# Optimization experiments

Hardware: AMD Instinct MI355X
Metric: run time of the kernel (lower is better)

## Reference

```python
import jax, jax.numpy as jnp
import numpy as np

H = 64        # hidden_dim
A = 21        # N_ACTIONS
B = 262144    # batch size


def setup_inputs() -> dict:
    key = jax.random.key(0)
    ks = jax.random.split(key, 32)

    def w(k, shape):
        fan_in = shape[0]
        return (jax.random.normal(k, shape, jnp.float32) / np.float32(np.sqrt(fan_in)))

    inp = {
        "x": jax.random.normal(ks[0], (B, 2, 2), jnp.float32),
        "b_act1": jax.random.randint(ks[1], (B,), 0, A),
        "b_act2": jax.random.randint(ks[2], (B,), 0, A),
        # enc: Linear(2,H), ReLU, Linear(H,H), ReLU
        "enc_w1": w(ks[3], (2, H)), "enc_b1": jnp.zeros((H,), jnp.float32),
        "enc_w2": w(ks[4], (H, H)), "enc_b2": jnp.zeros((H,), jnp.float32),
        # q_net: Linear(H,H), ReLU, Linear(H,A)
        "q_w1": w(ks[5], (H, H)), "q_b1": jnp.zeros((H,), jnp.float32),
        "q_w2": w(ks[6], (H, A)), "q_b2": jnp.zeros((A,), jnp.float32),
        # v_net: Linear(H,H), ReLU, Linear(H,1)
        "v_w1": w(ks[7], (H, H)), "v_b1": jnp.zeros((H,), jnp.float32),
        "v_w2": w(ks[8], (H, 1)), "v_b2": jnp.zeros((1,), jnp.float32),
        # lin2: Linear(H+A,H), ReLU, Linear(H,H), ReLU, Linear(H,H)
        "l2_w1": w(ks[9], (H + A, H)), "l2_b1": jnp.zeros((H,), jnp.float32),
        "l2_w2": w(ks[10], (H, H)), "l2_b2": jnp.zeros((H,), jnp.float32),
        "l2_w3": w(ks[11], (H, H)), "l2_b3": jnp.zeros((H,), jnp.float32),
        # lin3, lin4
        "l3_w": w(ks[12], (H, H)), "l3_b": jnp.zeros((H,), jnp.float32),
        "l4_w": w(ks[13], (H, A)), "l4_b": jnp.zeros((A,), jnp.float32),
        # q_prime_net: Linear(H,2H) ELU Linear(2H,H) ELU Linear(H,H) ELU Linear(H,1)
        "qp_w1": w(ks[14], (H, 2 * H)), "qp_b1": jnp.zeros((2 * H,), jnp.float32),
        "qp_w2": w(ks[15], (2 * H, H)), "qp_b2": jnp.zeros((H,), jnp.float32),
        "qp_w3": w(ks[16], (H, H)), "qp_b3": jnp.zeros((H,), jnp.float32),
        "qp_w4": w(ks[17], (H, 1)), "qp_b4": jnp.zeros((1,), jnp.float32),
    }
    return inp


def reference(x, b_act1, b_act2,
              enc_w1, enc_b1, enc_w2, enc_b2,
              q_w1, q_b1, q_w2, q_b2,
              v_w1, v_b1, v_w2, v_b2,
              l2_w1, l2_b1, l2_w2, l2_b2, l2_w3, l2_b3,
              l3_w, l3_b, l4_w, l4_b,
              qp_w1, qp_b1, qp_w2, qp_b2, qp_w3, qp_b3, qp_w4, qp_b4):
    relu = jax.nn.relu
    elu = jax.nn.elu

    def enc(z):
        return relu(relu(z @ enc_w1 + enc_b1) @ enc_w2 + enc_b2)

    def q_net(h):
        return relu(h @ q_w1 + q_b1) @ q_w2 + q_b2

    def lin2(e):  # ends with bare Linear (no final activation)
        h = relu(e @ l2_w1 + l2_b1)
        h = relu(h @ l2_w2 + l2_b2)
        return h @ l2_w3 + l2_b3

    def q_prime(z):
        h = elu(z @ qp_w1 + qp_b1)
        h = elu(h @ qp_w2 + qp_b2)
        h = elu(h @ qp_w3 + qp_b3)
        return h @ qp_w4 + qp_b4

    h1 = enc(x[:, 0, :])  # [B,H]
    h2 = enc(x[:, 1, :])
    q1, q2 = q_net(h1), q_net(h2)              # [B,A]
    key2 = jnp.stack([h1, h2], axis=1)          # [B,2,H]
    vtot = relu((h1 + h2) @ v_w1 + v_b1) @ v_w2 + v_b2  # [B,1]

    def joint(act1, act2):
        oh1 = jax.nn.one_hot(act1, A, dtype=h1.dtype)
        oh2 = jax.nn.one_hot(act2, A, dtype=h2.dtype)
        e = jnp.stack([jnp.concatenate([h1, oh1], axis=-1),
                       jnp.concatenate([h2, oh2], axis=-1)], axis=1)  # [B,2,H+A]
        key1 = lin2(e)                              # [B,2,H]
        q = q_prime(key1.mean(axis=1))              # [B,1]
        return key1, q

    key1, joint_qs = joint(b_act1, b_act2)
    a1_max = jnp.argmax(q1, axis=1)
    a2_max = jnp.argmax(q2, axis=1)
    key1_max, joint_max_qs = joint(a1_max, a2_max)

    def q_jt(k1):
        z = key2 + k1.mean(axis=1, keepdims=True) - k1 / 2  # [B,2,H]
        return relu(z @ l3_w + l3_b) @ l4_w + l4_b           # [B,2,A]

    q_jt_alt = q_jt(key1)
    q_jt_max_alt = q_jt(key1_max)

    return (q1, q2, joint_qs, joint_max_qs, vtot, q_jt_alt, q_jt_max_alt)
```

## Files before the change

### kernel.cpp

```cpp
#include <hip/hip_runtime.h>
#include <hip/hip_bf16.h>


#define B_TOT 262144

typedef __bf16 bf16_t;
typedef __bf16 bf16x4 __attribute__((ext_vector_type(4)));
typedef __bf16 bf16x8 __attribute__((ext_vector_type(8)));
typedef float  f32x2  __attribute__((ext_vector_type(2)));
typedef float  f32x4  __attribute__((ext_vector_type(4)));

#define MFMA16(a, b, c) __builtin_amdgcn_mfma_f32_16x16x32_bf16((a), (b), (c), 0, 0, 0)

enum : int {
  OFF_VW1  = 0,
  OFF_L2W1 = 4096,
  OFF_L2W2 = 8192,
  OFF_L2W3 = 12288,
  OFF_L3W  = 16384,
  OFF_L4W  = 20480,
  OFF_QP1  = 22528,
  OFF_QP2  = 30720,
  OFF_QP3  = 38912,
  WS_ELEMS = 43008
};
#define WS_BYTES (WS_ELEMS * 2)

enum : int {
  O_Q1   = 0,
  O_Q2   = 21 * B_TOT,
  O_JQ   = 42 * B_TOT,
  O_JMQ  = 43 * B_TOT,
  O_VT   = 44 * B_TOT,
  O_QJT  = 45 * B_TOT,
  O_QJTM = 87 * B_TOT
};

struct RDesc { const float* src; int K; int N; int NT; int off; };
struct RPack { RDesc d[9]; };

__global__ void repack_kernel(RPack P, bf16_t* __restrict__ ws) {
  RDesc d = P.d[blockIdx.x];
  int n = (d.K >> 5) * d.NT * 512;
  for (int i = threadIdx.x; i < n; i += blockDim.x) {
    int j  = i & 7;
    int l  = (i >> 3) & 63;
    int t  = i >> 9;
    int nt = t % d.NT;
    int kc = t / d.NT;
    int sk = kc * 32 + 16 * (j >> 2) + 4 * (l >> 4) + (j & 3);
    int sn = nt * 16 + (l & 15);
    float v = (sn < d.N) ? d.src[sk * d.N + sn] : 0.0f;
    ws[d.off + i] = (bf16_t)v;
  }
}

struct Args {
  const float* x; const int* a1; const int* a2;
  const float* ew1; const float* eb1; const float* ew2; const float* eb2;
  const float* qw1; const float* qb1; const float* qw2; const float* qb2;
  const float* vw1; const float* vb1; const float* vw2; const float* vb2;
  const float* l2w1; const float* l2b1; const float* l2w2; const float* l2b2;
  const float* l2w3; const float* l2b3;
  const float* l3w;  const float* l3b;  const float* l4w;  const float* l4b;
  const float* qpw1; const float* qpb1; const float* qpw2; const float* qpb2;
  const float* qpw3; const float* qpb3; const float* qpw4; const float* qpb4;
  float* out; const bf16_t* ws;
};

struct __align__(16) SMem {
  bf16_t h1b[64 * 72];
  bf16_t h2b[64 * 72];
  unsigned char scr[34816];
  float  bias[768];
  bf16_t oneh[21 * 68];
  int    acts[128];
  int    amax[128];
  float  red[64][2];
  int    redi[64][2];
};

__device__ __forceinline__ float eluf(float x) { return x > 0.f ? x : expm1f(x); }

__device__ __forceinline__ void fcA64(const float* __restrict__ fin, float* __restrict__ fout,
                                      const float* __restrict__ W, const float* __restrict__ Bv,
                                      bf16_t* hb, int r, int g) {
  f32x2 acc[8];
  const f32x2* Bv2 = (const f32x2*)(Bv + g * 16);
#pragma unroll
  for (int i = 0; i < 8; i++) acc[i] = Bv2[i];
#pragma unroll 4
  for (int k4 = 0; k4 < 16; k4++) {
    float4 a = *(const float4*)(fin + r * 68 + k4 * 4);
    float av[4] = {a.x, a.y, a.z, a.w};
#pragma unroll
    for (int kk = 0; kk < 4; kk++) {
      const f32x2* wr = (const f32x2*)(W + (k4 * 4 + kk) * 64 + g * 16);
      f32x2 avv = {av[kk], av[kk]};
#pragma unroll
      for (int i = 0; i < 8; i++) acc[i] += avv * wr[i];
    }
  }
#pragma unroll
  for (int i = 0; i < 8; i++) {
    float v0 = fmaxf(acc[i][0], 0.f), v1 = fmaxf(acc[i][1], 0.f);
    f32x2 v = {v0, v1};
    *(f32x2*)(fout + r * 68 + g * 16 + 2 * i) = v;
    if (hb) {
      hb[r * 72 + g * 16 + 2 * i]     = (bf16_t)v0;
      hb[r * 72 + g * 16 + 2 * i + 1] = (bf16_t)v1;
    }
  }
}

template <int NC>
__device__ __forceinline__ void qn2(const float* __restrict__ fin, const float* __restrict__ W21,
                                    const float* __restrict__ Bv, float* __restrict__ qo,
                                    int r, int colbase, float& bv, int& bi) {
  float acc[NC];
#pragma unroll
  for (int i = 0; i < NC; i++) acc[i] = Bv[colbase + i];
  for (int k4 = 0; k4 < 16; k4++) {
    float4 a = *(const float4*)(fin + r * 68 + k4 * 4);
    float av[4] = {a.x, a.y, a.z, a.w};
#pragma unroll
    for (int kk = 0; kk < 4; kk++) {
      const float* wr = W21 + (k4 * 4 + kk) * 21 + colbase;
#pragma unroll
      for (int i = 0; i < NC; i++) acc[i] = fmaf(av[kk], wr[i], acc[i]);
    }
  }
  bv = -3e38f; bi = 0;
#pragma unroll
  for (int i = 0; i < NC; i++) {
    qo[i] = acc[i];
    if (acc[i] > bv) { bv = acc[i]; bi = colbase + i; }
  }
}

template <bool USEWS, int NT, int KC>
__device__ __forceinline__ f32x4 tileT(const bf16x8* __restrict__ WF,
                                       const float* __restrict__ Wp, int N, int woff,
                                       const bf16x8* __restrict__ bin,
                                       const float* __restrict__ bias, int bbase,
                                       int nt, int l, int c, int u) {
  f32x4 a = *(const f32x4*)(bias + bbase + nt * 16 + 4 * u);
#pragma unroll
  for (int kc = 0; kc < KC; kc++) {
    bf16x8 w;
    if constexpr (USEWS) {
      w = WF[(woff >> 3) + (kc * NT + nt) * 64 + l];
    } else {
      int sn = nt * 16 + c;
      if (sn < N) {
#pragma unroll
        for (int j = 0; j < 8; j++)
          w[j] = (bf16_t)Wp[(kc * 32 + 16 * (j >> 2) + 4 * u + (j & 3)) * N + sn];
      } else {
#pragma unroll
        for (int j = 0; j < 8; j++) w[j] = (bf16_t)0.0f;
      }
    }
    a = MFMA16(w, bin[kc], a);
  }
  return a;
}

template <int MODE>
__device__ __forceinline__ bf16x8 pack2(f32x4 t0, f32x4 t1) {
  bf16x8 r;
#pragma unroll
  for (int j = 0; j < 8; j++) {
    float v = (j >> 2) ? t1[j & 3] : t0[j & 3];
    if constexpr (MODE == 1) v = fmaxf(v, 0.f);
    if constexpr (MODE == 2) v = eluf(v);
    r[j] = (bf16_t)v;
  }
  return r;
}

template <bool USEWS>
__global__ __launch_bounds__(256, 2) void qtran_main(Args A) {
  __shared__ SMem sm;
  const int t = threadIdx.x;
  const int wgbase = blockIdx.x * 64;
  const int r = t & 63;
  const int g = __builtin_amdgcn_readfirstlane(t >> 6);

  float* f0 = (float*)sm.scr;
  float* f1 = f0 + 64 * 68;

  if (t < 64) {
    sm.bias[t]        = A.vb1[t];
    sm.bias[64 + t]   = A.l2b1[t];
    sm.bias[128 + t]  = A.l2b2[t];
    sm.bias[192 + t]  = A.l2b3[t];
    sm.bias[384 + t]  = A.qpb2[t];
    sm.bias[448 + t]  = A.qpb3[t];
    sm.bias[512 + t]  = A.l3b[t];
    sm.bias[608 + t]  = A.vw2[t];
    sm.bias[672 + t]  = A.qpw4[t];
    sm.acts[t]        = A.a1[wgbase + t];
    sm.acts[64 + t]   = A.a2[wgbase + t];
  } else if (t < 192) {
    sm.bias[256 + t - 64] = A.qpb1[t - 64];
  } else if (t < 224) {
    int i = t - 192;
    sm.bias[576 + i] = (i < 21) ? A.l4b[i] : 0.0f;
  } else if (t == 224) {
    sm.bias[736] = A.vb2[0];
    sm.bias[737] = A.qpb4[0];
  }
  for (int i = t; i < 21 * 68; i += 256) {
    int a_ = i / 68, n_ = i % 68;
    sm.oneh[i] = (bf16_t)((n_ < 64) ? A.l2w1[(64 + a_) * 64 + n_] : 0.0f);
  }

  const int rowg = wgbase + r;
  float4 xv = ((const float4*)A.x)[rowg];
#pragma unroll 1
  for (int s = 0; s < 2; ++s) {
    float xa = s ? xv.z : xv.x;
    float xb = s ? xv.w : xv.y;
#pragma unroll
    for (int cc = 0; cc < 16; cc++) {
      int col = g * 16 + cc;
      float h = fmaf(xa, A.ew1[col], fmaf(xb, A.ew1[64 + col], A.eb1[col]));
      f0[r * 68 + col] = fmaxf(h, 0.f);
    }
    __syncthreads();
    fcA64(f0, f1, A.ew2, A.eb2, s ? sm.h2b : sm.h1b, r, g);
    __syncthreads();
    fcA64(f1, f0, A.qw1, A.qb1, nullptr, r, g);
    __syncthreads();
    {
      float* qo = A.out + (s ? O_Q2 : O_Q1) + rowg * 21;
      float bv; int bi;
      if (g == 0) {
        qn2<16>(f0, A.qw2, A.qb2, qo, r, 0, bv, bi);
        sm.red[r][0] = bv; sm.redi[r][0] = bi;
      } else if (g == 1) {
        qn2<5>(f0, A.qw2, A.qb2, qo + 16, r, 16, bv, bi);
        sm.red[r][1] = bv; sm.redi[r][1] = bi;
      }
    }
    __syncthreads();
    if (t < 64)
      sm.amax[s * 64 + t] = (sm.red[t][0] >= sm.red[t][1]) ? sm.redi[t][0] : sm.redi[t][1];
    __syncthreads();
  }
  __syncthreads();

  const int l = t & 63;
  const int c = l & 15, u = l >> 4;
  const int rb = g * 16;
  const int row = rb + c;
  float* out = A.out;
  const bf16x8* WF = (const bf16x8*)A.ws;
  const float* bias = sm.bias;
  float* S = (float*)sm.scr;

  auto HG = [&](const bf16_t* __restrict__ HB, int kc) -> bf16x8 {
    const bf16_t* p = HB + row * 72 + kc * 32 + 4 * u;
    bf16x4 lo = *(const bf16x4*)p;
    bf16x4 hi = *(const bf16x4*)(p + 16);
    bf16x8 rr;
#pragma unroll
    for (int d = 0; d < 4; d++) { rr[d] = lo[d]; rr[4 + d] = hi[d]; }
    return rr;
  };

  {
    bf16x8 aS[2];
#pragma unroll
    for (int kc = 0; kc < 2; kc++) {
      bf16x8 a1 = HG(sm.h1b, kc), a2 = HG(sm.h2b, kc);
      bf16x8 s8;
#pragma unroll
      for (int i = 0; i < 8; i++) s8[i] = (bf16_t)((float)a1[i] + (float)a2[i]);
      aS[kc] = s8;
    }
    float pr = 0.f;
#pragma unroll
    for (int nt = 0; nt < 4; nt++) {
      f32x4 tv = tileT<USEWS, 4, 2>(WF, A.vw1, 64, OFF_VW1, aS, bias, 0, nt, l, c, u);
      f32x4 wv = *(const f32x4*)(bias + 608 + nt * 16 + 4 * u);
#pragma unroll
      for (int p = 0; p < 4; p++) pr += fmaxf(tv[p], 0.f) * wv[p];
    }
    pr += __shfl_xor(pr, 16, 64);
    pr += __shfl_xor(pr, 32, 64);
    if (u == 0) out[O_VT + wgbase + row] = pr + bias[736];
  }

  const int* actsrc[2] = {sm.acts, sm.amax};
  bf16x8 k1f[2][2][2];
  f32x4 msum[2][4];

#pragma unroll
  for (int j = 0; j < 2; j++) {
    const bf16_t* HB = j ? sm.h2b : sm.h1b;
    bf16x8 bh[2];
#pragma unroll
    for (int kc = 0; kc < 2; kc++) bh[kc] = HG(HB, kc);
    f32x4 tS[4];
#pragma unroll
    for (int nt = 0; nt < 4; nt++)
      tS[nt] = tileT<USEWS, 4, 2>(WF, A.l2w1, 64, OFF_L2W1, bh, bias, 64, nt, l, c, u);
    bf16x8 b1[2][2];
#pragma unroll
    for (int x = 0; x < 2; x++) {
      const int act = actsrc[x][j * 64 + row];
      f32x4 tt0 = tS[0], tt1 = tS[1], tt2 = tS[2], tt3 = tS[3];
      bf16x4 oh0 = *(const bf16x4*)(sm.oneh + act * 68 + 0 * 16 + 4 * u);
      bf16x4 oh1 = *(const bf16x4*)(sm.oneh + act * 68 + 1 * 16 + 4 * u);
      bf16x4 oh2 = *(const bf16x4*)(sm.oneh + act * 68 + 2 * 16 + 4 * u);
      bf16x4 oh3 = *(const bf16x4*)(sm.oneh + act * 68 + 3 * 16 + 4 * u);
#pragma unroll
      for (int p = 0; p < 4; p++) {
        tt0[p] += (float)oh0[p]; tt1[p] += (float)oh1[p];
        tt2[p] += (float)oh2[p]; tt3[p] += (float)oh3[p];
      }
      b1[x][0] = pack2<1>(tt0, tt1);
      b1[x][1] = pack2<1>(tt2, tt3);
    }
    bf16x8 b2[2][2];
#pragma unroll
    for (int x = 0; x < 2; x++)
#pragma unroll
      for (int f = 0; f < 2; f++) {
        f32x4 t0 = tileT<USEWS, 4, 2>(WF, A.l2w2, 64, OFF_L2W2, b1[x], bias, 128, 2 * f, l, c, u);
        f32x4 t1 = tileT<USEWS, 4, 2>(WF, A.l2w2, 64, OFF_L2W2, b1[x], bias, 128, 2 * f + 1, l, c, u);
        b2[x][f] = pack2<1>(t0, t1);
      }
#pragma unroll
    for (int x = 0; x < 2; x++)
#pragma unroll
      for (int f = 0; f < 2; f++) {
        f32x4 t0 = tileT<USEWS, 4, 2>(WF, A.l2w3, 64, OFF_L2W3, b2[x], bias, 192, 2 * f, l, c, u);
        f32x4 t1 = tileT<USEWS, 4, 2>(WF, A.l2w3, 64, OFF_L2W3, b2[x], bias, 192, 2 * f + 1, l, c, u);
        k1f[x][j][f] = pack2<0>(t0, t1);
        if (j == 0) { msum[x][2 * f] = t0; msum[x][2 * f + 1] = t1; }
        else        { msum[x][2 * f] += t0; msum[x][2 * f + 1] += t1; }
      }
  }

#pragma unroll
  for (int j = 0; j < 2; j++) {
    const bf16_t* HB = j ? sm.h2b : sm.h1b;
    bf16x8 h8[2];
#pragma unroll
    for (int kc = 0; kc < 2; kc++) h8[kc] = HG(HB, kc);
#pragma unroll
    for (int x = 0; x < 2; x++) {
      bf16x8 aZ[2];
#pragma unroll
      for (int kc = 0; kc < 2; kc++) {
        bf16x8 kk = k1f[x][1 - j][kc];
#pragma unroll
        for (int i = 0; i < 8; i++)
          aZ[kc][i] = (bf16_t)((float)h8[kc][i] + 0.5f * (float)kk[i]);
      }
      bf16x8 bz[2];
#pragma unroll
      for (int f = 0; f < 2; f++) {
        f32x4 t0 = tileT<USEWS, 4, 2>(WF, A.l3w, 64, OFF_L3W, aZ, bias, 512, 2 * f, l, c, u);
        f32x4 t1 = tileT<USEWS, 4, 2>(WF, A.l3w, 64, OFF_L3W, aZ, bias, 512, 2 * f + 1, l, c, u);
        bz[f] = pack2<1>(t0, t1);
      }
#pragma unroll
      for (int nt = 0; nt < 2; nt++) {
        f32x4 tq = tileT<USEWS, 2, 2>(WF, A.l4w, 21, OFF_L4W, bz, bias, 576, nt, l, c, u);
#pragma unroll
        for (int p = 0; p < 4; p++) {
          int n2 = nt * 16 + 4 * u + p;
          if (n2 < 21) S[x * 2752 + row * 43 + j * 21 + n2] = tq[p];
        }
      }
    }
  }

  {
    bf16x8 aM[2][2];
#pragma unroll
    for (int x = 0; x < 2; x++)
#pragma unroll
      for (int kc = 0; kc < 2; kc++) {
        f32x4 m0 = 0.5f * msum[x][2 * kc], m1 = 0.5f * msum[x][2 * kc + 1];
        aM[x][kc] = pack2<0>(m0, m1);
      }
    bf16x8 bq[2][4];
#pragma unroll
    for (int x = 0; x < 2; x++)
#pragma unroll
      for (int f = 0; f < 4; f++) {
        f32x4 t0 = tileT<USEWS, 8, 2>(WF, A.qpw1, 128, OFF_QP1, aM[x], bias, 256, 2 * f, l, c, u);
        f32x4 t1 = tileT<USEWS, 8, 2>(WF, A.qpw1, 128, OFF_QP1, aM[x], bias, 256, 2 * f + 1, l, c, u);
        bq[x][f] = pack2<2>(t0, t1);
      }
    bf16x8 b3[2][2];
#pragma unroll
    for (int x = 0; x < 2; x++)
#pragma unroll
      for (int f = 0; f < 2; f++) {
        f32x4 t0 = tileT<USEWS, 4, 4>(WF, A.qpw2, 64, OFF_QP2, bq[x], bias, 384, 2 * f, l, c, u);
        f32x4 t1 = tileT<USEWS, 4, 4>(WF, A.qpw2, 64, OFF_QP2, bq[x], bias, 384, 2 * f + 1, l, c, u);
        b3[x][f] = pack2<2>(t0, t1);
      }
    float pj[2] = {0.f, 0.f};
#pragma unroll
    for (int x = 0; x < 2; x++)
#pragma unroll
      for (int nt = 0; nt < 4; nt++) {
        f32x4 tq = tileT<USEWS, 4, 2>(WF, A.qpw3, 64, OFF_QP3, b3[x], bias, 448, nt, l, c, u);
        f32x4 w4 = *(const f32x4*)(bias + 672 + nt * 16 + 4 * u);
#pragma unroll
        for (int p = 0; p < 4; p++) pj[x] += eluf(tq[p]) * w4[p];
      }
#pragma unroll
    for (int x = 0; x < 2; x++) {
      float v = pj[x];
      v += __shfl_xor(v, 16, 64);
      v += __shfl_xor(v, 32, 64);
      if (u == 0) out[(x ? O_JMQ : O_JQ) + wgbase + row] = v + bias[737];
    }
  }

#pragma unroll
  for (int x = 0; x < 2; x++) {
    const int ob = (x ? O_QJTM : O_QJT) + (wgbase + rb) * 42;
    const float* Sx = S + x * 2752 + rb * 43;
    for (int i2 = l; i2 < 672; i2 += 64)
      out[ob + i2] = Sx[(i2 / 42) * 43 + (i2 % 42)];
  }
}

extern "C" void kernel_launch(void* const* d_in, const int* in_sizes, int n_in,
                              void* d_out, int out_size, void* d_ws, size_t ws_size,
                              hipStream_t stream) {
  (void)in_sizes; (void)n_in; (void)out_size;
  Args A;
  A.x    = (const float*)d_in[0];
  A.a1   = (const int*)d_in[1];
  A.a2   = (const int*)d_in[2];
  A.ew1  = (const float*)d_in[3];
  A.eb1  = (const float*)d_in[4];
  A.ew2  = (const float*)d_in[5];
  A.eb2  = (const float*)d_in[6];
  A.qw1  = (const float*)d_in[7];
  A.qb1  = (const float*)d_in[8];
  A.qw2  = (const float*)d_in[9];
  A.qb2  = (const float*)d_in[10];
  A.vw1  = (const float*)d_in[11];
  A.vb1  = (const float*)d_in[12];
  A.vw2  = (const float*)d_in[13];
  A.vb2  = (const float*)d_in[14];
  A.l2w1 = (const float*)d_in[15];
  A.l2b1 = (const float*)d_in[16];
  A.l2w2 = (const float*)d_in[17];
  A.l2b2 = (const float*)d_in[18];
  A.l2w3 = (const float*)d_in[19];
  A.l2b3 = (const float*)d_in[20];
  A.l3w  = (const float*)d_in[21];
  A.l3b  = (const float*)d_in[22];
  A.l4w  = (const float*)d_in[23];
  A.l4b  = (const float*)d_in[24];
  A.qpw1 = (const float*)d_in[25];
  A.qpb1 = (const float*)d_in[26];
  A.qpw2 = (const float*)d_in[27];
  A.qpb2 = (const float*)d_in[28];
  A.qpw3 = (const float*)d_in[29];
  A.qpb3 = (const float*)d_in[30];
  A.qpw4 = (const float*)d_in[31];
  A.qpb4 = (const float*)d_in[32];
  A.out  = (float*)d_out;
  A.ws   = (const bf16_t*)d_ws;

  if (ws_size >= (size_t)WS_BYTES) {
    bf16_t* ws = (bf16_t*)d_ws;
    RPack P;
    P.d[0] = {A.vw1,  64, 64,  4, OFF_VW1};
    P.d[1] = {A.l2w1, 64, 64,  4, OFF_L2W1};
    P.d[2] = {A.l2w2, 64, 64,  4, OFF_L2W2};
    P.d[3] = {A.l2w3, 64, 64,  4, OFF_L2W3};
    P.d[4] = {A.l3w,  64, 64,  4, OFF_L3W};
    P.d[5] = {A.l4w,  64, 21,  2, OFF_L4W};
    P.d[6] = {A.qpw1, 64, 128, 8, OFF_QP1};
    P.d[7] = {A.qpw2, 128, 64, 4, OFF_QP2};
    P.d[8] = {A.qpw3, 64, 64,  4, OFF_QP3};
    hipLaunchKernelGGL(repack_kernel, dim3(9), dim3(256), 0, stream, P, ws);
    hipLaunchKernelGGL(HIP_KERNEL_NAME(qtran_main<true>), dim3(B_TOT / 64), dim3(256), 0,
                       stream, A);
  } else {
    hipLaunchKernelGGL(HIP_KERNEL_NAME(qtran_main<false>), dim3(B_TOT / 64), dim3(256), 0,
                       stream, A);
  }
}
```

Measured before the change: 908.0 us.

## Shrink LDS footprint and raise occupancy to four workgroups per CU

Cuts shared memory by running the encoder/q-net FC layers in place in one float buffer (stride 66), tightening the bf16 hidden buffers to stride 68, and dropping the LDS one-hot table in favour of direct global reads of l2_w1 rows. The q_jt output staging is reordered so each x pass writes out before the next, which halves the S scratch. The launch bound is raised to 4 blocks per CU so more waves can hide latency. In exchange, the in-place FC adds extra barriers and register staging, and the tighter register budget may cause spills.

```diff
diff --git a/kernel.cpp b/kernel.cpp
--- a/kernel.cpp
+++ b/kernel.cpp
@@ -69,11 +69,10 @@
 };
 
 struct __align__(16) SMem {
-  bf16_t h1b[64 * 72];
-  bf16_t h2b[64 * 72];
-  unsigned char scr[34816];
+  unsigned char scr[16896];
+  bf16_t h1b[64 * 68];
+  bf16_t h2b[64 * 68];
   float  bias[768];
-  bf16_t oneh[21 * 68];
   int    acts[128];
   int    amax[128];
   float  red[64][2];
@@ -82,35 +81,45 @@
 
 __device__ __forceinline__ float eluf(float x) { return x > 0.f ? x : expm1f(x); }
 
-__device__ __forceinline__ void fcA64(const float* __restrict__ fin, float* __restrict__ fout,
-                                      const float* __restrict__ W, const float* __restrict__ Bv,
-                                      bf16_t* hb, int r, int g) {
+__device__ __forceinline__ void fcA64ip(float* __restrict__ f,
+                                        const float* __restrict__ W,
+                                        const float* __restrict__ Bv,
+                                        bf16_t* __restrict__ hb, int r, int g) {
   f32x2 acc[8];
   const f32x2* Bv2 = (const f32x2*)(Bv + g * 16);
 #pragma unroll
   for (int i = 0; i < 8; i++) acc[i] = Bv2[i];
+  const f32x2* fr = (const f32x2*)(f + r * 66);
+#pragma unroll 1
+  for (int hh = 0; hh < 2; hh++) {
+    f32x2 in[16];
+#pragma unroll
+    for (int i = 0; i < 16; i++) in[i] = fr[16 * hh + i];
 #pragma unroll 4
-  for (int k4 = 0; k4 < 16; k4++) {
-    float4 a = *(const float4*)(fin + r * 68 + k4 * 4);
-    float av[4] = {a.x, a.y, a.z, a.w};
-#pragma unroll
-    for (int kk = 0; kk < 4; kk++) {
-      const f32x2* wr = (const f32x2*)(W + (k4 * 4 + kk) * 64 + g * 16);
-      f32x2 avv = {av[kk], av[kk]};
-#pragma unroll
-      for (int i = 0; i < 8; i++) acc[i] += avv * wr[i];
-    }
-  }
+    for (int k2 = 0; k2 < 16; k2++) {
+      int k = 32 * hh + 2 * k2;
+      const f32x2* wr0 = (const f32x2*)(W + k * 64 + g * 16);
+      const f32x2* wr1 = (const f32x2*)(W + (k + 1) * 64 + g * 16);
+      f32x2 a0 = {in[k2][0], in[k2][0]};
+      f32x2 a1 = {in[k2][1], in[k2][1]};
+#pragma unroll
+      for (int i = 0; i < 8; i++) acc[i] += a0 * wr0[i];
+#pragma unroll
+      for (int i = 0; i < 8; i++) acc[i] += a1 * wr1[i];
+    }
+  }
+  __syncthreads();
 #pragma unroll
   for (int i = 0; i < 8; i++) {
     float v0 = fmaxf(acc[i][0], 0.f), v1 = fmaxf(acc[i][1], 0.f);
     f32x2 v = {v0, v1};
-    *(f32x2*)(fout + r * 68 + g * 16 + 2 * i) = v;
+    *(f32x2*)(f + r * 66 + g * 16 + 2 * i) = v;
     if (hb) {
-      hb[r * 72 + g * 16 + 2 * i]     = (bf16_t)v0;
-      hb[r * 72 + g * 16 + 2 * i + 1] = (bf16_t)v1;
-    }
-  }
+      hb[r * 68 + g * 16 + 2 * i]     = (bf16_t)v0;
+      hb[r * 68 + g * 16 + 2 * i + 1] = (bf16_t)v1;
+    }
+  }
+  __syncthreads();
 }
 
 template <int NC>
@@ -120,15 +129,14 @@
   float acc[NC];
 #pragma unroll
   for (int i = 0; i < NC; i++) acc[i] = Bv[colbase + i];
-  for (int k4 = 0; k4 < 16; k4++) {
-    float4 a = *(const float4*)(fin + r * 68 + k4 * 4);
-    float av[4] = {a.x, a.y, a.z, a.w};
-#pragma unroll
-    for (int kk = 0; kk < 4; kk++) {
-      const float* wr = W21 + (k4 * 4 + kk) * 21 + colbase;
-#pragma unroll
-      for (int i = 0; i < NC; i++) acc[i] = fmaf(av[kk], wr[i], acc[i]);
-    }
+  for (int k2 = 0; k2 < 32; k2++) {
+    f32x2 a = *(const f32x2*)(fin + r * 66 + 2 * k2);
+    const float* wr0 = W21 + (2 * k2) * 21 + colbase;
+    const float* wr1 = W21 + (2 * k2 + 1) * 21 + colbase;
+#pragma unroll
+    for (int i = 0; i < NC; i++) acc[i] = fmaf(a[0], wr0[i], acc[i]);
+#pragma unroll
+    for (int i = 0; i < NC; i++) acc[i] = fmaf(a[1], wr1[i], acc[i]);
   }
   bv = -3e38f; bi = 0;
 #pragma unroll
@@ -180,7 +188,7 @@
 }
 
 template <bool USEWS>
-__global__ __launch_bounds__(256, 2) void qtran_main(Args A) {
+__global__ __launch_bounds__(256, 4) void qtran_main(Args A) {
   __shared__ SMem sm;
   const int t = threadIdx.x;
   const int wgbase = blockIdx.x * 64;
@@ -188,7 +196,6 @@
   const int g = __builtin_amdgcn_readfirstlane(t >> 6);
 
   float* f0 = (float*)sm.scr;
-  float* f1 = f0 + 64 * 68;
 
   if (t < 64) {
     sm.bias[t]        = A.vb1[t];
@@ -211,10 +218,6 @@
     sm.bias[736] = A.vb2[0];
     sm.bias[737] = A.qpb4[0];
   }
-  for (int i = t; i < 21 * 68; i += 256) {
-    int a_ = i / 68, n_ = i % 68;
-    sm.oneh[i] = (bf16_t)((n_ < 64) ? A.l2w1[(64 + a_) * 64 + n_] : 0.0f);
-  }
 
   const int rowg = wgbase + r;
   float4 xv = ((const float4*)A.x)[rowg];
@@ -223,16 +226,16 @@
     float xa = s ? xv.z : xv.x;
     float xb = s ? xv.w : xv.y;
 #pragma unroll
-    for (int cc = 0; cc < 16; cc++) {
+    for (int cc = 0; cc < 16; cc += 2) {
       int col = g * 16 + cc;
-      float h = fmaf(xa, A.ew1[col], fmaf(xb, A.ew1[64 + col], A.eb1[col]));
-      f0[r * 68 + col] = fmaxf(h, 0.f);
+      float h0 = fmaf(xa, A.ew1[col],     fmaf(xb, A.ew1[64 + col],     A.eb1[col]));
+      float h1 = fmaf(xa, A.ew1[col + 1], fmaf(xb, A.ew1[64 + col + 1], A.eb1[col + 1]));
+      f32x2 v = {fmaxf(h0, 0.f), fmaxf(h1, 0.f)};
+      *(f32x2*)(f0 + r * 66 + col) = v;
     }
     __syncthreads();
-    fcA64(f0, f1, A.ew2, A.eb2, s ? sm.h2b : sm.h1b, r, g);
-    __syncthreads();
-    fcA64(f1, f0, A.qw1, A.qb1, nullptr, r, g);
-    __syncthreads();
+    fcA64ip(f0, A.ew2, A.eb2, s ? sm.h2b : sm.h1b, r, g);
+    fcA64ip(f0, A.qw1, A.qb1, nullptr, r, g);
     {
       float* qo = A.out + (s ? O_Q2 : O_Q1) + rowg * 21;
       float bv; int bi;
@@ -249,7 +252,6 @@
       sm.amax[s * 64 + t] = (sm.red[t][0] >= sm.red[t][1]) ? sm.redi[t][0] : sm.redi[t][1];
     __syncthreads();
   }
-  __syncthreads();
 
   const int l = t & 63;
   const int c = l & 15, u = l >> 4;
@@ -261,7 +263,7 @@
   float* S = (float*)sm.scr;
 
   auto HG = [&](const bf16_t* __restrict__ HB, int kc) -> bf16x8 {
-    const bf16_t* p = HB + row * 72 + kc * 32 + 4 * u;
+    const bf16_t* p = HB + row * 68 + kc * 32 + 4 * u;
     bf16x4 lo = *(const bf16x4*)p;
     bf16x4 hi = *(const bf16x4*)(p + 16);
     bf16x8 rr;
@@ -311,16 +313,11 @@
 #pragma unroll
     for (int x = 0; x < 2; x++) {
       const int act = actsrc[x][j * 64 + row];
-      f32x4 tt0 = tS[0], tt1 = tS[1], tt2 = tS[2], tt3 = tS[3];
-      bf16x4 oh0 = *(const bf16x4*)(sm.oneh + act * 68 + 0 * 16 + 4 * u);
-      bf16x4 oh1 = *(const bf16x4*)(sm.oneh + act * 68 + 1 * 16 + 4 * u);
-      bf16x4 oh2 = *(const bf16x4*)(sm.oneh + act * 68 + 2 * 16 + 4 * u);
-      bf16x4 oh3 = *(const bf16x4*)(sm.oneh + act * 68 + 3 * 16 + 4 * u);
-#pragma unroll
-      for (int p = 0; p < 4; p++) {
-        tt0[p] += (float)oh0[p]; tt1[p] += (float)oh1[p];
-        tt2[p] += (float)oh2[p]; tt3[p] += (float)oh3[p];
-      }
+      const float* ohp = A.l2w1 + (64 + act) * 64 + 4 * u;
+      f32x4 tt0 = tS[0] + *(const f32x4*)(ohp);
+      f32x4 tt1 = tS[1] + *(const f32x4*)(ohp + 16);
+      f32x4 tt2 = tS[2] + *(const f32x4*)(ohp + 32);
+      f32x4 tt3 = tS[3] + *(const f32x4*)(ohp + 48);
       b1[x][0] = pack2<1>(tt0, tt1);
       b1[x][1] = pack2<1>(tt2, tt3);
     }
@@ -346,20 +343,18 @@
   }
 
 #pragma unroll
-  for (int j = 0; j < 2; j++) {
-    const bf16_t* HB = j ? sm.h2b : sm.h1b;
-    bf16x8 h8[2];
-#pragma unroll
-    for (int kc = 0; kc < 2; kc++) h8[kc] = HG(HB, kc);
-#pragma unroll
-    for (int x = 0; x < 2; x++) {
+  for (int x = 0; x < 2; x++) {
+#pragma unroll
+    for (int j = 0; j < 2; j++) {
+      const bf16_t* HB = j ? sm.h2b : sm.h1b;
       bf16x8 aZ[2];
 #pragma unroll
       for (int kc = 0; kc < 2; kc++) {
+        bf16x8 h8 = HG(HB, kc);
         bf16x8 kk = k1f[x][1 - j][kc];
 #pragma unroll
         for (int i = 0; i < 8; i++)
-          aZ[kc][i] = (bf16_t)((float)h8[kc][i] + 0.5f * (float)kk[i]);
+          aZ[kc][i] = (bf16_t)((float)h8[i] + 0.5f * (float)kk[i]);
       }
       bf16x8 bz[2];
 #pragma unroll
@@ -374,10 +369,14 @@
 #pragma unroll
         for (int p = 0; p < 4; p++) {
           int n2 = nt * 16 + 4 * u + p;
-          if (n2 < 21) S[x * 2752 + row * 43 + j * 21 + n2] = tq[p];
+          if (n2 < 21) S[row * 43 + j * 21 + n2] = tq[p];
         }
       }
     }
+    const int ob = (x ? O_QJTM : O_QJT) + (wgbase + rb) * 42;
+    const float* Sx = S + rb * 43;
+    for (int i2 = l; i2 < 672; i2 += 64)
+      out[ob + i2] = Sx[(i2 / 42) * 43 + (i2 % 42)];
   }
 
   {
@@ -424,14 +423,6 @@
       v += __shfl_xor(v, 32, 64);
       if (u == 0) out[(x ? O_JMQ : O_JQ) + wgbase + row] = v + bias[737];
     }
-  }
-
-#pragma unroll
-  for (int x = 0; x < 2; x++) {
-    const int ob = (x ? O_QJTM : O_QJT) + (wgbase + rb) * 42;
-    const float* Sx = S + x * 2752 + rb * 43;
-    for (int i2 = l; i2 < 672; i2 += 64)
-      out[ob + i2] = Sx[(i2 / 42) * 43 + (i2 % 42)];
   }
 }
 
```

New measurement: 977.8 us. 7.7% more time.
